# Kernel tuning notes

Hardware: AMD Instinct MI355X
Metric: run time of the kernel (lower is better)

Reference implementation:

```python
import jax, jax.numpy as jnp
import numpy as np

B, C, G = 32768, 17, 7  # batch, channels (1 obj + 4 box + 12 class), grid


def setup_inputs() -> dict:
    key = jax.random.key(0)
    k1, k2, k3 = jax.random.split(key, 3)
    # Predictions: uniform in (0,1) so sqrt of wh channels is well-defined.
    out = jax.random.uniform(k1, (B, C, G, G), dtype=jnp.float32, minval=1e-4, maxval=1.0)
    # remaining channels uniform in (0,1).
    label = jax.random.uniform(k2, (B, C, G, G), dtype=jnp.float32, minval=1e-4, maxval=1.0)
    obj = (jax.random.uniform(k3, (B, 1, G, G)) < 0.3).astype(jnp.float32)
    label = label.at[:, 0:1].set(obj)
    return {"out": out, "label": label}


def reference(out, label):
    # objectness channel
    d0 = label[:, 0] - out[:, 0]                      # [B,7,7]
    noobj_loss = 0.5 * d0 ** 2
    # object-present branch
    loc_loss = jnp.sum((label[:, 1:3] - out[:, 1:3]) ** 2, axis=1)                       # [B,7,7]
    size_loss = jnp.sum((jnp.sqrt(label[:, 3:5]) - jnp.sqrt(out[:, 3:5])) ** 2, axis=1)  # [B,7,7]
    prob_loss = d0 ** 2
    class_loss = jnp.sum((label[:, 5:17] - out[:, 5:17]) ** 2, axis=1)                   # [B,7,7]
    obj_loss = 5.0 * (loc_loss + size_loss) + prob_loss + class_loss
    cell_loss = jnp.where(label[:, 0] == 0, noobj_loss, obj_loss)
    return jnp.sum(cell_loss) / (out.shape[0] * 49)
```

## Files before the change

kernel.cpp:

```cpp
#include <hip/hip_runtime.h>


#define BPC   833
#define CELLS 49
#define NTOT  (32768 * BPC)
#define N4    (NTOT / 4)
#define NBLK  2048

__global__ __launch_bounds__(256) void yolo_partial(const float* __restrict__ outp,
                                                    const float* __restrict__ lab,
                                                    float* __restrict__ partial) {
    __shared__ uint2 lut[BPC];
    for (int r = threadIdx.x; r < BPC; r += 256) {
        const int c    = r / CELLS;
        const int cell = r - c * CELLS;
        unsigned wa, wb;
        if (c == 0)      { wa = 0x3F00u; wb = 0x3F00u; }
        else if (c <= 4) { wa = 0x0000u; wb = 0x40A0u; }
        else             { wa = 0x0000u; wb = 0x3F80u; }
        const bool sq = (c == 3) || (c == 4);
        lut[r].x = (wa << 16) | wb;
        lut[r].y = (unsigned)cell | (sq ? 0x100u : 0u);
    }
    __syncthreads();

    const int tid    = blockIdx.x * 256 + threadIdx.x;
    const int stride = gridDim.x * 256;
    float acc = 0.0f;

    for (int i4 = tid; i4 < N4; i4 += stride) {
        const float4 o4 = reinterpret_cast<const float4*>(outp)[i4];
        const float4 l4 = reinterpret_cast<const float4*>(lab)[i4];
        const float ov[4] = {o4.x, o4.y, o4.z, o4.w};
        const float lv[4] = {l4.x, l4.y, l4.z, l4.w};

        const unsigned idx   = (unsigned)i4 * 4u;
        const unsigned b     = idx / 833u;
        const unsigned bbase = b * 833u;
        const unsigned r0    = idx - bbase;

#pragma unroll
        for (int j = 0; j < 4; ++j) {
            const unsigned rj   = r0 + j;
            const unsigned wrap = (rj >= 833u) ? 833u : 0u;
            const unsigned r    = rj - wrap;
            const uint2 e = lut[r];
            const float  a  = __uint_as_float(e.x & 0xFFFF0000u);
            const float  bw = __uint_as_float(e.x << 16);
            const unsigned cell = e.y & 0xFFu;
            const float m  = lab[bbase + wrap + cell];
            const float o1 = ov[j], l1 = lv[j];
            const float dl = l1 - o1;
            const float dq = sqrtf(l1) - sqrtf(o1);
            const float d  = (e.y >= 0x100u) ? dq : dl;
            acc += d * d * fmaf(bw, m, a);
        }
    }

#pragma unroll
    for (int off = 32; off > 0; off >>= 1)
        acc += __shfl_down(acc, off, 64);

    __shared__ float wsum[4];
    const int lane = threadIdx.x & 63;
    const int wid  = threadIdx.x >> 6;
    if (lane == 0) wsum[wid] = acc;
    __syncthreads();
    if (threadIdx.x == 0)
        partial[blockIdx.x] = wsum[0] + wsum[1] + wsum[2] + wsum[3];
}

__global__ __launch_bounds__(256) void yolo_final(const float* __restrict__ partial,
                                                  float* __restrict__ outv) {
    float acc = 0.0f;
    for (int i = threadIdx.x; i < NBLK; i += 256) acc += partial[i];
#pragma unroll
    for (int off = 32; off > 0; off >>= 1)
        acc += __shfl_down(acc, off, 64);

    __shared__ float wsum[4];
    const int lane = threadIdx.x & 63;
    const int wid  = threadIdx.x >> 6;
    if (lane == 0) wsum[wid] = acc;
    __syncthreads();
    if (threadIdx.x == 0)
        outv[0] = (wsum[0] + wsum[1] + wsum[2] + wsum[3]) * (1.0f / 1605632.0f);
}

extern "C" void kernel_launch(void* const* d_in, const int* in_sizes, int n_in,
                              void* d_out, int out_size, void* d_ws, size_t ws_size,
                              hipStream_t stream) {
    const float* outp = (const float*)d_in[0];
    const float* lab  = (const float*)d_in[1];
    float* partial    = (float*)d_ws;
    float* res        = (float*)d_out;

    yolo_partial<<<NBLK, 256, 0, stream>>>(outp, lab, partial);
    yolo_final<<<1, 256, 0, stream>>>(partial, res);
}
```

Baseline: 44.21 us.

## Fuse final reduction into main kernel via last-block counter; simplify per-element math

Drops the separate final-reduce kernel. Each block now bumps an atomic counter after writing its partial sum, and the last block to finish sums all partials and writes the result. A hipMemsetAsync resets the counter on every call. The shared lookup table is split into two arrays with three padded wrap-around entries, which removes the per-element wrap test. The squared sqrt difference is rewritten as l+o-2*sqrt(l*o), so each element needs one sqrt instead of two. The block count also changes slightly. The kernel is likely bandwidth-bound, so the compute savings may matter little, and the memset adds its own small launch.

```diff
diff --git a/kernel.cpp b/kernel.cpp
--- a/kernel.cpp
+++ b/kernel.cpp
@@ -5,22 +5,30 @@
 #define CELLS 49
 #define NTOT  (32768 * BPC)
 #define N4    (NTOT / 4)
-#define NBLK  2048
+#define NBLK  2040
 
-__global__ __launch_bounds__(256) void yolo_partial(const float* __restrict__ outp,
-                                                    const float* __restrict__ lab,
-                                                    float* __restrict__ partial) {
-    __shared__ uint2 lut[BPC];
-    for (int r = threadIdx.x; r < BPC; r += 256) {
-        const int c    = r / CELLS;
-        const int cell = r - c * CELLS;
-        unsigned wa, wb;
-        if (c == 0)      { wa = 0x3F00u; wb = 0x3F00u; }
-        else if (c <= 4) { wa = 0x0000u; wb = 0x40A0u; }
-        else             { wa = 0x0000u; wb = 0x3F80u; }
-        const bool sq = (c == 3) || (c == 4);
-        lut[r].x = (wa << 16) | wb;
-        lut[r].y = (unsigned)cell | (sq ? 0x100u : 0u);
+__global__ __launch_bounds__(256) void yolo_loss(const float* __restrict__ outp,
+                                                 const float* __restrict__ lab,
+                                                 float* __restrict__ partial,
+                                                 unsigned* __restrict__ ctr,
+                                                 float* __restrict__ res) {
+    __shared__ unsigned lutW[836];
+    __shared__ unsigned lutO[836];
+    for (int r = threadIdx.x; r < 836; r += 256) {
+        unsigned w, o;
+        if (r >= 833) {
+            w = (0x3F00u << 16) | 0x3F00u;
+            o = (unsigned)r;
+        } else {
+            const int c    = r / CELLS;
+            const int cell = r - c * CELLS;
+            if (c == 0)      w = (0x3F00u << 16) | 0x3F00u;
+            else if (c <= 4) w = 0x40A0u;
+            else             w = 0x3F80u;
+            o = (unsigned)cell | ((c == 3 || c == 4) ? 0x80000000u : 0u);
+        }
+        lutW[r] = w;
+        lutO[r] = o;
     }
     __syncthreads();
 
@@ -41,19 +49,17 @@
 
 #pragma unroll
         for (int j = 0; j < 4; ++j) {
-            const unsigned rj   = r0 + j;
-            const unsigned wrap = (rj >= 833u) ? 833u : 0u;
-            const unsigned r    = rj - wrap;
-            const uint2 e = lut[r];
-            const float  a  = __uint_as_float(e.x & 0xFFFF0000u);
-            const float  bw = __uint_as_float(e.x << 16);
-            const unsigned cell = e.y & 0xFFu;
-            const float m  = lab[bbase + wrap + cell];
-            const float o1 = ov[j], l1 = lv[j];
-            const float dl = l1 - o1;
-            const float dq = sqrtf(l1) - sqrtf(o1);
-            const float d  = (e.y >= 0x100u) ? dq : dl;
-            acc += d * d * fmaf(bw, m, a);
+            const unsigned wp = lutW[r0 + j];
+            const unsigned op = lutO[r0 + j];
+            const float a  = __uint_as_float(wp & 0xFFFF0000u);
+            const float bw = __uint_as_float(wp << 16);
+            const float m  = lab[bbase + (op & 0x3FFu)];
+            const float l1 = lv[j], o1 = ov[j];
+            const float dl  = l1 - o1;
+            const float dl2 = dl * dl;
+            const float q2  = (l1 + o1) - 2.0f * __builtin_amdgcn_sqrtf(l1 * o1);
+            const float d2  = ((int)op < 0) ? q2 : dl2;
+            acc = fmaf(fmaf(bw, m, a), d2, acc);
         }
     }
 
@@ -66,25 +72,28 @@
     const int wid  = threadIdx.x >> 6;
     if (lane == 0) wsum[wid] = acc;
     __syncthreads();
-    if (threadIdx.x == 0)
+
+    __shared__ int isLast;
+    if (threadIdx.x == 0) {
         partial[blockIdx.x] = wsum[0] + wsum[1] + wsum[2] + wsum[3];
-}
+        __threadfence();
+        isLast = (atomicAdd(ctr, 1u) == (unsigned)(gridDim.x - 1));
+    }
+    __syncthreads();
 
-__global__ __launch_bounds__(256) void yolo_final(const float* __restrict__ partial,
-                                                  float* __restrict__ outv) {
-    float acc = 0.0f;
-    for (int i = threadIdx.x; i < NBLK; i += 256) acc += partial[i];
+    if (isLast) {
+        __threadfence();
+        float s = 0.0f;
+        for (int i = threadIdx.x; i < NBLK; i += 256)
+            s += partial[i];
 #pragma unroll
-    for (int off = 32; off > 0; off >>= 1)
-        acc += __shfl_down(acc, off, 64);
-
-    __shared__ float wsum[4];
-    const int lane = threadIdx.x & 63;
-    const int wid  = threadIdx.x >> 6;
-    if (lane == 0) wsum[wid] = acc;
-    __syncthreads();
-    if (threadIdx.x == 0)
-        outv[0] = (wsum[0] + wsum[1] + wsum[2] + wsum[3]) * (1.0f / 1605632.0f);
+        for (int off = 32; off > 0; off >>= 1)
+            s += __shfl_down(s, off, 64);
+        if (lane == 0) wsum[wid] = s;
+        __syncthreads();
+        if (threadIdx.x == 0)
+            res[0] = (wsum[0] + wsum[1] + wsum[2] + wsum[3]) * (1.0f / 1605632.0f);
+    }
 }
 
 extern "C" void kernel_launch(void* const* d_in, const int* in_sizes, int n_in,
@@ -93,8 +102,9 @@
     const float* outp = (const float*)d_in[0];
     const float* lab  = (const float*)d_in[1];
     float* partial    = (float*)d_ws;
+    unsigned* ctr     = (unsigned*)((char*)d_ws + NBLK * sizeof(float));
     float* res        = (float*)d_out;
 
-    yolo_partial<<<NBLK, 256, 0, stream>>>(outp, lab, partial);
-    yolo_final<<<1, 256, 0, stream>>>(partial, res);
+    hipMemsetAsync(ctr, 0, sizeof(unsigned), stream);
+    yolo_loss<<<NBLK, 256, 0, stream>>>(outp, lab, partial, ctr, res);
 }
```

New measurement: 109.7 us. 148% more time.
